# Performance work log

Measured on AMD Instinct MI355X. Metric: run time of the kernel, lower is better.

Reference implementation:

```python
import jax, jax.numpy as jnp
import numpy as np

G = 8           # graphs
NBG = 1024      # blocks per graph
APB = 4         # atoms per block
NC = 1          # coord channels
HID = 512
ES = 64
K = 9
L = 3
NLVL = 50
NB = G * NBG
NU = NB * APB
NUM_BLOCK, NUM_ATOM, NUM_POS = 25, 16, 16
BIG = 1e9


def _cumsum_ids(seg_lengths, n):
    # faithful to torch: zeros, mark segment starts via cumsum(lengths)[:-1], cumsum
    ids = jnp.zeros((n,), jnp.int32).at[jnp.cumsum(seg_lengths)[:-1]].set(1)
    return jnp.cumsum(ids)


def setup_inputs() -> dict:
    key = jax.random.key(0)
    ks = jax.random.split(key, 18)
    s = 0.02
    return {
        'Z': 3.0 * jax.random.normal(ks[0], (NU, NC, 3), jnp.float32),
        'B': jax.random.randint(ks[1], (NB,), 0, NUM_BLOCK),
        'A': jax.random.randint(ks[2], (NU,), 0, NUM_ATOM),
        'atom_positions': jax.random.randint(ks[3], (NU,), 0, NUM_POS),
        'block_lengths': jnp.full((NB,), APB, jnp.int32),
        'lengths': jnp.full((G,), NBG, jnp.int32),
        'segment_ids': jax.random.randint(ks[4], (NB,), 0, 2),
        'noise': jax.random.normal(ks[5], (NU, NC, 3), jnp.float32),
        'noise_level': jax.random.randint(ks[6], (G,), 0, NLVL),
        'sigmas': jnp.asarray(np.exp(np.linspace(np.log(10.0), np.log(0.01), NLVL)), jnp.float32),
        'atom_emb': s * jax.random.normal(ks[7], (NUM_ATOM, HID), jnp.float32),
        'pos_emb': s * jax.random.normal(ks[8], (NUM_POS, HID), jnp.float32),
        'block_emb': s * jax.random.normal(ks[9], (NUM_BLOCK, HID), jnp.float32),
        'edge_emb': s * jax.random.normal(ks[10], (2, ES), jnp.float32),
        'Wm': s * jax.random.normal(ks[11], (L, HID, HID), jnp.float32),
        'We': s * jax.random.normal(ks[12], (L, ES, HID), jnp.float32),
        'Wu': s * jax.random.normal(ks[13], (L, HID, HID), jnp.float32),
        'wz': s * jax.random.normal(ks[14], (L, HID), jnp.float32),
        'W1': s * jax.random.normal(ks[15], (HID, HID), jnp.float32),
        'b1': jnp.zeros((HID,), jnp.float32),
        'W2': s * jax.random.normal(ks[16], (HID, 1), jnp.float32),
    }


def _forward(Z, B, A, atom_positions, block_lengths, lengths, segment_ids,
             noise, noise_level, sigmas, atom_emb, pos_emb, block_emb, edge_emb,
             Wm, We, Wu, wz, W1, b1, W2):
    nb, nu, g = B.shape[0], A.shape[0], lengths.shape[0]
    nbg, apb = nb // g, nu // nb
    batch_id = _cumsum_ids(lengths, nb)        # [Nb]
    block_id = _cumsum_ids(block_lengths, nu)  # [Nu]

    # perturb: Z + noise * sigma[noise_level[graph]]
    used = sigmas[noise_level][batch_id][block_id]          # [Nu]
    Zp = Z + noise * used[:, None, None]                    # [Nu, NC, 3]

    # block embedding: atom + position + block-type
    H0 = atom_emb[A] + pos_emb[atom_positions] + block_emb[B][block_id]  # [Nu, H]

    # edges: fully connect -> split intra/inter by segment -> knn by min atom-pair distance
    xa = Zp.reshape(g, nbg * apb * NC, 3)
    sq = jnp.sum(xa * xa, axis=-1)
    d2 = sq[:, :, None] + sq[:, None, :] - 2.0 * jnp.einsum('gnd,gmd->gnm', xa, xa)
    D = d2.reshape(g, nbg, apb * NC, nbg, apb * NC).min(axis=(2, 4))     # [g, nbg, nbg]
    seg = segment_ids.reshape(g, nbg)
    same = seg[:, :, None] == seg[:, None, :]
    eye = jnp.eye(nbg, dtype=bool)[None]
    _, idx_intra = jax.lax.top_k(-jnp.where(same & ~eye, D, BIG), K)     # [g, nbg, K]
    _, idx_inter = jax.lax.top_k(-jnp.where(~same, D, BIG), K)
    off = (jnp.arange(g, dtype=jnp.int32) * nbg)[:, None, None]
    dst_loc = jnp.broadcast_to(jnp.arange(nbg, dtype=jnp.int32)[None, :, None] + off, (g, nbg, K))
    src = jnp.concatenate([(idx_intra + off).reshape(-1), (idx_inter + off).reshape(-1)])
    dst = jnp.concatenate([dst_loc.reshape(-1), dst_loc.reshape(-1)])
    eattr = edge_emb[jnp.concatenate([jnp.zeros(g * nbg * K, jnp.int32), jnp.ones(g * nbg * K, jnp.int32)])]

    # encoder (GET surrogate): block-level equivariant message passing
    h = jax.ops.segment_sum(H0, block_id, num_segments=nb) / apb                    # [Nb, H]
    Zb0 = jax.ops.segment_sum(Zp.mean(axis=1), block_id, num_segments=nb) / apb    # [Nb, 3]
    Zb = Zb0
    for l in range(Wm.shape[0]):
        m = jax.nn.silu((h[src] + h[dst]) @ Wm[l] + eattr @ We[l])                  # [E, H]
        h = h + jax.nn.silu(jax.ops.segment_sum(m, dst, num_segments=nb) @ Wu[l])
        coef = jnp.tanh(m @ wz[l])                                                  # [E]
        Zb = Zb + jax.ops.segment_sum((Zb[src] - Zb[dst]) * coef[:, None], dst, num_segments=nb) / (2 * K)
    pred_Z = Zp + (Zb - Zb0)[block_id][:, None, :]
    unit_repr = H0 + h[block_id]
    block_repr = h
    graph_repr = jax.ops.segment_sum(h, batch_id, num_segments=g)

    # energy head: SiLU -> Linear -> SiLU -> Linear(no bias), summed per graph
    e = jax.nn.silu(jax.nn.silu(block_repr) @ W1 + b1) @ W2                         # [Nb, 1]
    pred_energy = jax.ops.segment_sum(e[:, 0], batch_id, num_segments=g)            # [g]

    pred_noise = pred_Z - Zp
    per_unit = jnp.sum((pred_noise - noise) ** 2, axis=(-1, -2))                    # [Nu]
    nl = jax.ops.segment_sum(per_unit, batch_id[block_id], num_segments=g)
    loss = 0.5 * nl.mean()
    return pred_energy, pred_noise, unit_repr, block_repr, graph_repr, loss


def reference(Z, B, A, atom_positions, block_lengths, lengths, segment_ids,
              noise, noise_level, sigmas, atom_emb, pos_emb, block_emb, edge_emb,
              Wm, We, Wu, wz, W1, b1, W2):
    return _forward(Z, B, A, atom_positions, block_lengths, lengths, segment_ids,
                    noise, noise_level, sigmas, atom_emb, pos_emb, block_emb, edge_emb,
                    Wm, We, Wu, wz, W1, b1, W2)
```

## Files before the change

kernel.cpp:

```cpp
#include <hip/hip_runtime.h>
#include <hip/hip_bf16.h>

typedef __bf16 bf16;
typedef __bf16 bf16x2 __attribute__((ext_vector_type(2)));
typedef __bf16 bf16x8 __attribute__((ext_vector_type(8)));
typedef float floatx4 __attribute__((ext_vector_type(4)));
typedef float floatx2 __attribute__((ext_vector_type(2)));

__device__ __forceinline__ float silu_f(float x) {
    float e = __expf(-x);
    return x * __builtin_amdgcn_rcpf(1.0f + e);
}

__device__ __forceinline__ float2 unpack_bf2(unsigned v) {
    float2 r;
    r.x = __uint_as_float(v << 16);
    r.y = __uint_as_float(v & 0xFFFF0000u);
    return r;
}

__device__ __forceinline__ void unpack8(const bf16* p, float* o) {
    uint4 u = *(const uint4*)p;
    float2 a = unpack_bf2(u.x); o[0]=a.x; o[1]=a.y;
    float2 b = unpack_bf2(u.y); o[2]=b.x; o[3]=b.y;
    float2 c = unpack_bf2(u.z); o[4]=c.x; o[5]=c.y;
    float2 d = unpack_bf2(u.w); o[6]=d.x; o[7]=d.y;
}

__device__ __forceinline__ void gll16(const bf16* g, bf16* l) {
    __builtin_amdgcn_global_load_lds((const __attribute__((address_space(1))) void*)g,
                                     (__attribute__((address_space(3))) void*)l, 16, 0, 0);
}

__global__ __launch_bounds__(256) void init_kernel(
    const float* __restrict__ Z, const float* __restrict__ noise,
    const int* __restrict__ nl, const float* __restrict__ sig,
    const int* __restrict__ Aarr, const int* __restrict__ posa, const int* __restrict__ Barr,
    const float* __restrict__ atom_emb, const float* __restrict__ pos_emb,
    const float* __restrict__ block_emb,
    const float* __restrict__ Wm,
    float* __restrict__ Zp, float* __restrict__ Zb0, float* __restrict__ Zb,
    float* __restrict__ hf, bf16* __restrict__ hb,
    bf16* __restrict__ WmT)
{
    __shared__ float zsh[12];
    __shared__ float tile[32][33];
    int bid = blockIdx.x, tid = threadIdx.x;
    if (bid < 8192) {
        int b = bid, g = b >> 10;
        if (tid < 12) {
            float sg = sig[nl[g]];
            int idx = b*12 + tid;
            float zp = Z[idx] + noise[idx]*sg;
            Zp[idx] = zp;
            zsh[tid] = zp;
        }
        __syncthreads();
        if (tid < 3) {
            float v = 0.25f*(zsh[tid] + zsh[3+tid] + zsh[6+tid] + zsh[9+tid]);
            Zb0[b*3+tid] = v; Zb[b*3+tid] = v;
        }
        int ai[4], pi[4];
        #pragma unroll
        for (int a = 0; a < 4; a++) { ai[a] = Aarr[b*4+a]*512; pi[a] = posa[b*4+a]*512; }
        int bb = Barr[b]*512;
        #pragma unroll
        for (int cc = 0; cc < 2; cc++) {
            int c = tid + cc*256;
            float s = 0.0f;
            #pragma unroll
            for (int a = 0; a < 4; a++) s += atom_emb[ai[a]+c] + pos_emb[pi[a]+c];
            s = 0.25f*s + block_emb[bb+c];
            hf[(size_t)b*512+c] = s;
            hb[(size_t)b*512+c] = (bf16)s;
        }
        return;
    }
    int rem = bid - 8192;
    int bx = rem & 15, by = rem >> 4;
    int tx = tid & 31, ty = tid >> 5;
    #pragma unroll
    for (int i = 0; i < 32; i += 8)
        tile[ty+i][tx] = Wm[(size_t)(by*32+ty+i)*512 + bx*32+tx];
    __syncthreads();
    #pragma unroll
    for (int i = 0; i < 32; i += 8)
        WmT[(size_t)(bx*32+ty+i)*512 + by*32+tx] = (bf16)tile[tx][ty+i];
}

__device__ void knn_body(int kb, const float* __restrict__ Zp, const int* __restrict__ seg,
                         int* __restrict__ nbr) {
    int wid = threadIdx.x >> 6;
    int lane = threadIdx.x & 63;
    int r = ((kb & 7) << 10) + ((kb >> 3) << 2) + wid;
    int g = r >> 10;
    int il = r & 1023;
    int base = g << 10;
    int segr = seg[r];
    float za[4][3];
    #pragma unroll
    for (int a = 0; a < 4; a++)
        #pragma unroll
        for (int d = 0; d < 3; d++)
            za[a][d] = Zp[r*12 + a*3 + d];
    floatx2 ax[4], ay[4], az[4];
    #pragma unroll
    for (int a = 0; a < 4; a++) {
        ax[a] = (floatx2){za[a][0], za[a][0]};
        ay[a] = (floatx2){za[a][1], za[a][1]};
        az[a] = (floatx2){za[a][2], za[a][2]};
    }
    float dist[16];
    unsigned smask = 0;
    #pragma unroll
    for (int t = 0; t < 16; t++) {
        int jb = base + t*64 + lane;
        const float4* p = (const float4*)(Zp + (size_t)jb*12);
        float4 v0 = p[0], v1 = p[1], v2 = p[2];
        floatx2 bx0 = {v0.x, v0.w}, by0 = {v0.y, v1.x}, bz0 = {v0.z, v1.y};
        floatx2 bx1 = {v1.z, v2.y}, by1 = {v1.w, v2.z}, bz1 = {v2.x, v2.w};
        floatx2 mn = {3.0e38f, 3.0e38f};
        #pragma unroll
        for (int a = 0; a < 4; a++) {
            floatx2 dx = ax[a] - bx0, dy = ay[a] - by0, dz = az[a] - bz0;
            floatx2 dd = dx*dx + dy*dy + dz*dz;
            mn.x = fminf(mn.x, dd.x); mn.y = fminf(mn.y, dd.y);
            dx = ax[a] - bx1; dy = ay[a] - by1; dz = az[a] - bz1;
            dd = dx*dx + dy*dy + dz*dz;
            mn.x = fminf(mn.x, dd.x); mn.y = fminf(mn.y, dd.y);
        }
        dist[t] = fminf(mn.x, mn.y);
        if (seg[jb] == segr) smask |= (1u << t);
    }
    const float INF = 3.0e38f;
    for (int phase = 0; phase < 2; phase++) {
        float wd[16];
        #pragma unroll
        for (int t = 0; t < 16; t++) {
            bool ok = (phase == 0) ? (((smask >> t) & 1u) && (t*64 + lane != il))
                                   : (!((smask >> t) & 1u));
            wd[t] = ok ? dist[t] : INF;
        }
        for (int it = 0; it < 9; it++) {
            float bd = wd[0]; int bt = 0;
            #pragma unroll
            for (int t = 1; t < 16; t++) { if (wd[t] < bd) { bd = wd[t]; bt = t; } }
            float mv = bd;
            #pragma unroll
            for (int off = 32; off >= 1; off >>= 1) mv = fminf(mv, __shfl_xor(mv, off, 64));
            unsigned long long msk = __ballot(bd == mv);
            int wl = __ffsll(msk) - 1;
            int wt = __shfl(bt, wl, 64);
            if (lane == 0) nbr[r*18 + phase*9 + it] = base + wt*64 + wl;
            bool amwin = (lane == wl);
            #pragma unroll
            for (int t = 0; t < 16; t++) if (amwin && t == wt) wd[t] = INF;
        }
    }
}

template<int PIPE>
__device__ void gemm_body(const bf16* __restrict__ A, const bf16* __restrict__ BT,
                          bf16* __restrict__ Pb, float* __restrict__ hf,
                          bf16* __restrict__ hb, bf16* __restrict__ shp,
                          const float* __restrict__ b1, const float* __restrict__ W2,
                          float* __restrict__ out_e,
                          float* __restrict__ Zb, const float* __restrict__ zacc,
                          const float* __restrict__ Zb0, const float* __restrict__ noise,
                          float* __restrict__ out_pn, float* __restrict__ out_loss,
                          float* __restrict__ out_gr,
                          int mode, int bid)
{
    constexpr int NBUF = PIPE ? 3 : 1;
    __shared__ alignas(16) bf16 sA[NBUF*128*32];
    __shared__ alignas(16) bf16 sB[NBUF*64*32];
    __shared__ float grbuf[4][32];
    __shared__ float lsh[4];
    __shared__ float ered[4];
    int mt = bid & 63, nt = bid >> 6;
    int m0 = mt*128, n0 = nt*64;
    int tid = threadIdx.x, lane = tid & 63, w = tid >> 6;
    int wm = w & 1, wn = w >> 1;
    int lm = lane & 15, q = lane >> 4;

    int pA0 = w*128 + lane, pA1 = pA0 + 64, pB = w*64 + lane;
    int rA0 = pA0 >> 2, qA0 = (pA0 & 3) ^ ((rA0 >> 1) & 3);
    int rA1 = pA1 >> 2, qA1 = (pA1 & 3) ^ ((rA1 >> 1) & 3);
    int rB  = pB  >> 2, qB  = (pB  & 3) ^ ((rB  >> 1) & 3);
    const bf16* gA0 = A  + (size_t)(m0 + rA0)*512 + qA0*8;
    const bf16* gA1 = A  + (size_t)(m0 + rA1)*512 + qA1*8;
    const bf16* gB  = BT + (size_t)(n0 + rB )*512 + qB*8;
    int dA0 = (w*128)*8, dA1 = (w*128 + 64)*8, dB = (w*64)*8;

    int swq = (q ^ ((lm >> 1) & 3)) * 8;
    int offA[4], offB[2];
    #pragma unroll
    for (int tm = 0; tm < 4; tm++) offA[tm] = (wm*64 + tm*16 + lm)*32 + swq;
    #pragma unroll
    for (int tn = 0; tn < 2; tn++) offB[tn] = (wn*32 + tn*16 + lm)*32 + swq;

    floatx4 zv = {0.0f, 0.0f, 0.0f, 0.0f};
    floatx4 acc[4][2];
    #pragma unroll
    for (int i = 0; i < 4; i++)
        #pragma unroll
        for (int j = 0; j < 2; j++) acc[i][j] = zv;

    if constexpr (PIPE == 0) {
        for (int k0 = 0; k0 < 512; k0 += 32) {
            gll16(gA0 + k0, sA + dA0);
            gll16(gA1 + k0, sA + dA1);
            gll16(gB  + k0, sB + dB);
            __syncthreads();
            bf16x8 af[4], bfr[2];
            #pragma unroll
            for (int tm = 0; tm < 4; tm++) af[tm] = *(const bf16x8*)(sA + offA[tm]);
            #pragma unroll
            for (int tn = 0; tn < 2; tn++) bfr[tn] = *(const bf16x8*)(sB + offB[tn]);
            #pragma unroll
            for (int tm = 0; tm < 4; tm++)
                #pragma unroll
                for (int tn = 0; tn < 2; tn++)
                    acc[tm][tn] = __builtin_amdgcn_mfma_f32_16x16x32_bf16(af[tm], bfr[tn], acc[tm][tn], 0, 0, 0);
            __syncthreads();
        }
    } else {
        gll16(gA0,      sA + dA0);
        gll16(gA1,      sA + dA1);
        gll16(gB,       sB + dB);
        gll16(gA0 + 32, sA + 4096 + dA0);
        gll16(gA1 + 32, sA + 4096 + dA1);
        gll16(gB  + 32, sB + 2048 + dB);
        #pragma unroll
        for (int t = 0; t < 16; t++) {
            const int cur = t % 3;
            if (t < 14) {
                const int k0 = (t + 2) * 32;
                const int nb = (t + 2) % 3;
                gll16(gA0 + k0, sA + nb*4096 + dA0);
                gll16(gA1 + k0, sA + nb*4096 + dA1);
                gll16(gB  + k0, sB + nb*2048 + dB);
                asm volatile("s_waitcnt vmcnt(6)" ::: "memory");
            } else if (t == 14) {
                asm volatile("s_waitcnt vmcnt(3)" ::: "memory");
            } else {
                asm volatile("s_waitcnt vmcnt(0)" ::: "memory");
            }
            __builtin_amdgcn_s_barrier();
            asm volatile("" ::: "memory");
            const bf16* a_ = sA + cur*4096;
            const bf16* b_ = sB + cur*2048;
            bf16x8 af[4], bfr[2];
            #pragma unroll
            for (int tm = 0; tm < 4; tm++) af[tm] = *(const bf16x8*)(a_ + offA[tm]);
            #pragma unroll
            for (int tn = 0; tn < 2; tn++) bfr[tn] = *(const bf16x8*)(b_ + offB[tn]);
            #pragma unroll
            for (int tm = 0; tm < 4; tm++)
                #pragma unroll
                for (int tn = 0; tn < 2; tn++)
                    acc[tm][tn] = __builtin_amdgcn_mfma_f32_16x16x32_bf16(af[tm], bfr[tn], acc[tm][tn], 0, 0, 0);
            asm volatile("" ::: "memory");
            __builtin_amdgcn_s_barrier();
        }
    }

    if (mode == 1 && nt == 0) {
        int o = m0*3 + tid;
        Zb[o] += zacc[o] * (1.0f/18.0f);
        if (tid < 128) {
            int o2 = m0*3 + 256 + tid;
            Zb[o2] += zacc[o2] * (1.0f/18.0f);
        }
    }

    if (mode == 2) {
        float esum = 0.0f;
        #pragma unroll
        for (int tn = 0; tn < 2; tn++) {
            int col = n0 + wn*32 + tn*16 + lm;
            float bb = b1[col];
            float w2 = W2[col];
            #pragma unroll
            for (int tm = 0; tm < 4; tm++)
                #pragma unroll
                for (int rr = 0; rr < 4; rr++)
                    esum += silu_f(acc[tm][tn][rr] + bb) * w2;
        }
        #pragma unroll
        for (int off = 32; off >= 1; off >>= 1) esum += __shfl_xor(esum, off, 64);
        if (lane == 0) ered[w] = esum;
        __syncthreads();
        if (tid == 0) {
            float tot = ered[0] + ered[1] + ered[2] + ered[3];
            atomicAdd(&out_e[m0 >> 10], tot);
        }
        return;
    }

    float colsum[2] = {0.0f, 0.0f};
    #pragma unroll
    for (int tm = 0; tm < 4; tm++) {
        #pragma unroll
        for (int tn = 0; tn < 2; tn++) {
            #pragma unroll
            for (int rr = 0; rr < 4; rr++) {
                int row = m0 + wm*64 + tm*16 + q*4 + rr;
                int col = n0 + wn*32 + tn*16 + lm;
                size_t o = (size_t)row*512 + col;
                float v = acc[tm][tn][rr];
                if (mode == 0) {
                    Pb[o] = (bf16)v;
                } else {
                    float nh = hf[o] + silu_f(v);
                    hf[o] = nh;
                    colsum[tn] += nh;
                    if (shp) shp[o] = (bf16)silu_f(nh);
                    else     hb[o] = (bf16)nh;
                }
            }
        }
    }

    if (mode == 1 && shp) {
        #pragma unroll
        for (int tn = 0; tn < 2; tn++) {
            float v = colsum[tn];
            v += __shfl_xor(v, 16, 64);
            v += __shfl_xor(v, 32, 64);
            if (q == 0) grbuf[w][tn*16 + lm] = v;
        }
        __syncthreads();
        if (((w & 1) == 0) && lane < 32) {
            float tot = grbuf[w][lane] + grbuf[w + 1][lane];
            int col = n0 + (w >> 1)*32 + lane;
            atomicAdd(&out_gr[(m0 >> 10)*512 + col], tot);
        }
        if (nt == 0) {
            float per2 = 0.0f;
            #pragma unroll
            for (int j = 0; j < 2; j++) {
                int u = m0*4 + tid*2 + j;
                int b = u >> 2;
                #pragma unroll
                for (int d = 0; d < 3; d++) {
                    float dv = Zb[b*3 + d] - Zb0[b*3 + d];
                    out_pn[(size_t)u*3 + d] = dv;
                    float e = dv - noise[(size_t)u*3 + d];
                    per2 += e*e;
                }
            }
            #pragma unroll
            for (int off = 32; off >= 1; off >>= 1) per2 += __shfl_xor(per2, off, 64);
            if (lane == 0) lsh[w] = per2;
            __syncthreads();
            if (tid == 0)
                atomicAdd(out_loss, (lsh[0]+lsh[1]+lsh[2]+lsh[3]) * (1.0f/16.0f));
        }
    }
}

template<int MODE>
__global__ __launch_bounds__(256) void gemm_mode_kernel(const bf16* __restrict__ A, const bf16* __restrict__ BT,
                                                        bf16* __restrict__ Pb, float* __restrict__ hf,
                                                        bf16* __restrict__ hb, bf16* __restrict__ shp,
                                                        const float* __restrict__ b1, const float* __restrict__ W2,
                                                        float* __restrict__ out_e,
                                                        float* __restrict__ Zb, const float* __restrict__ zacc,
                                                        const float* __restrict__ Zb0, const float* __restrict__ noise,
                                                        float* __restrict__ out_pn, float* __restrict__ out_loss,
                                                        float* __restrict__ out_gr) {
    gemm_body<1>(A, BT, Pb, hf, hb, shp, b1, W2, out_e, Zb, zacc,
                 Zb0, noise, out_pn, out_loss, out_gr, MODE, blockIdx.x);
}

__global__ __launch_bounds__(256) void knn_pgemm0_kernel(const bf16* __restrict__ hb,
                                                         const bf16* __restrict__ WmT,
                                                         bf16* __restrict__ Pb,
                                                         const float* __restrict__ Zp,
                                                         const int* __restrict__ seg,
                                                         int* __restrict__ nbr,
                                                         const float* __restrict__ Wm,
                                                         const float* __restrict__ Wu,
                                                         const float* __restrict__ W1,
                                                         bf16* __restrict__ WmTw,
                                                         bf16* __restrict__ WuT,
                                                         bf16* __restrict__ W1T,
                                                         const float* __restrict__ edge_emb,
                                                         const float* __restrict__ We,
                                                         float* __restrict__ ebias,
                                                         float* __restrict__ out_gr,
                                                         float* __restrict__ out_e,
                                                         float* __restrict__ out_loss) {
    __shared__ float ttile[32][33];
    int bid = blockIdx.x, tid = threadIdx.x;
    if (bid < 512) {
        gemm_body<0>(hb, WmT, Pb, nullptr, nullptr, nullptr, nullptr, nullptr, nullptr,
                     nullptr, nullptr, nullptr, nullptr, nullptr, nullptr, nullptr, 0, bid);
        return;
    }
    if (bid < 2560) {
        knn_body(bid - 512, Zp, seg, nbr);
        return;
    }
    int tb = bid - 2560;
    if (tb < 1536) {
        int z = 1 + (tb >> 8), rem = tb & 255;
        int bx = rem & 15, by = rem >> 4;
        int tx = tid & 31, ty = tid >> 5;
        const float* src; bf16* dst;
        if (z < 3)      { src = Wm + (size_t)z*262144;     dst = WmTw + (size_t)z*262144; }
        else if (z < 6) { src = Wu + (size_t)(z-3)*262144; dst = WuT + (size_t)(z-3)*262144; }
        else            { src = W1;                        dst = W1T; }
        #pragma unroll
        for (int i = 0; i < 32; i += 8)
            ttile[ty+i][tx] = src[(size_t)(by*32+ty+i)*512 + bx*32+tx];
        __syncthreads();
        #pragma unroll
        for (int i = 0; i < 32; i += 8)
            dst[(size_t)(bx*32+ty+i)*512 + by*32+tx] = (bf16)ttile[tx][ty+i];
        return;
    }
    tb -= 1536;
    if (tb < 12) {
        int gid = tb*256 + tid;
        int l = gid >> 10, t = (gid >> 9) & 1, c = gid & 511;
        float s = 0.0f;
        #pragma unroll 8
        for (int e = 0; e < 64; e++)
            s += edge_emb[t*64 + e] * We[(size_t)(l*64 + e)*512 + c];
        ebias[gid] = s;
        return;
    }
    tb -= 12;
    int k = tb*256 + tid;
    if (k < 4096) out_gr[k] = 0.0f;
    else if (k < 4104) out_e[k-4096] = 0.0f;
    else if (k == 4104) out_loss[0] = 0.0f;
}

__global__ __launch_bounds__(256) void edge_kernel(const bf16* __restrict__ Pb, const float* __restrict__ ebias,
                                                   const float* __restrict__ wz, const float* __restrict__ Zb,
                                                   const int* __restrict__ nbr, bf16* __restrict__ msum,
                                                   float* __restrict__ zacc) {
    int bid = blockIdx.x, tid = threadIdx.x;
    int lane = tid & 63, wid = tid >> 6;
    int b = ((bid & 7) << 10) | ((bid >> 3) << 2) | wid;
    __shared__ int srcs[4][18];
    if (tid < 72) {
        int w2 = tid / 18, e2 = tid - w2*18;
        int bb = ((bid & 7) << 10) | ((bid >> 3) << 2) | w2;
        srcs[w2][e2] = nbr[bb*18 + e2];
    }
    __syncthreads();
    int c0 = lane << 3;
    float pd[8], eb0[8], eb1[8], wv[8];
    unpack8(Pb + (size_t)b*512 + c0, pd);
    *(float4*)(eb0)   = *(const float4*)(ebias + c0);
    *(float4*)(eb0+4) = *(const float4*)(ebias + c0 + 4);
    *(float4*)(eb1)   = *(const float4*)(ebias + 512 + c0);
    *(float4*)(eb1+4) = *(const float4*)(ebias + 512 + c0 + 4);
    *(float4*)(wv)    = *(const float4*)(wz + c0);
    *(float4*)(wv+4)  = *(const float4*)(wz + c0 + 4);
    float ms[8];
    #pragma unroll
    for (int j = 0; j < 8; j++) ms[j] = 0.0f;
    float pdot[18];
    #pragma unroll
    for (int e = 0; e < 18; e++) {
        int s = srcs[wid][e];
        float pv[8];
        unpack8(Pb + (size_t)s*512 + c0, pv);
        float dot = 0.0f;
        #pragma unroll
        for (int j = 0; j < 8; j++) {
            float base = (e < 9) ? eb0[j] : eb1[j];
            float m = silu_f(pv[j] + pd[j] + base);
            ms[j] += m;
            dot += m * wv[j];
        }
        pdot[e] = dot;
    }
    bf16x8 mp;
    #pragma unroll
    for (int j = 0; j < 8; j++) mp[j] = (bf16)ms[j];
    *(bf16x8*)(msum + (size_t)b*512 + c0) = mp;
    #pragma unroll
    for (int e = 0; e < 18; e++) {
        float v = pdot[e];
        #pragma unroll
        for (int off = 32; off >= 1; off >>= 1) v += __shfl_xor(v, off, 64);
        pdot[e] = v;
    }
    float dotv = 0.0f;
    #pragma unroll
    for (int e = 0; e < 18; e++) dotv = (lane == e) ? pdot[e] : dotv;
    float coef = tanhf(dotv);
    float t3[3] = {0.0f, 0.0f, 0.0f};
    if (lane < 18) {
        int se = srcs[wid][lane];
        #pragma unroll
        for (int d = 0; d < 3; d++)
            t3[d] = (Zb[se*3 + d] - Zb[b*3 + d]) * coef;
    }
    #pragma unroll
    for (int off = 16; off >= 1; off >>= 1) {
        t3[0] += __shfl_xor(t3[0], off, 64);
        t3[1] += __shfl_xor(t3[1], off, 64);
        t3[2] += __shfl_xor(t3[2], off, 64);
    }
    if (lane == 0) {
        zacc[b*3 + 0] = t3[0];
        zacc[b*3 + 1] = t3[1];
        zacc[b*3 + 2] = t3[2];
    }
}

__global__ __launch_bounds__(256) void unitrepr_kernel(const int* __restrict__ Aarr, const int* __restrict__ posa,
                                                       const int* __restrict__ Barr,
                                                       const float* __restrict__ atom_emb, const float* __restrict__ pos_emb,
                                                       const float* __restrict__ block_emb,
                                                       const float* __restrict__ hf, float* __restrict__ out_ur) {
    int gid = blockIdx.x*256 + threadIdx.x;
    int u = gid >> 7, c = (gid & 127) << 2, b = u >> 2;
    float4 va = *(const float4*)(atom_emb + (size_t)Aarr[u]*512 + c);
    float4 vp = *(const float4*)(pos_emb + (size_t)posa[u]*512 + c);
    float4 vb = *(const float4*)(block_emb + (size_t)Barr[b]*512 + c);
    float4 vh = *(const float4*)(hf + (size_t)b*512 + c);
    float4 o;
    o.x = va.x + vp.x + vb.x + vh.x;
    o.y = va.y + vp.y + vb.y + vh.y;
    o.z = va.z + vp.z + vb.z + vh.z;
    o.w = va.w + vp.w + vb.w + vh.w;
    *(float4*)(out_ur + (size_t)u*512 + c) = o;
}

extern "C" void kernel_launch(void* const* d_in, const int* in_sizes, int n_in,
                              void* d_out, int out_size, void* d_ws, size_t ws_size,
                              hipStream_t stream) {
    const float* Z         = (const float*)d_in[0];
    const int*   B         = (const int*)d_in[1];
    const int*   A         = (const int*)d_in[2];
    const int*   ap        = (const int*)d_in[3];
    const int*   seg       = (const int*)d_in[6];
    const float* noise     = (const float*)d_in[7];
    const int*   nl        = (const int*)d_in[8];
    const float* sig       = (const float*)d_in[9];
    const float* atom_emb  = (const float*)d_in[10];
    const float* pos_emb   = (const float*)d_in[11];
    const float* block_emb = (const float*)d_in[12];
    const float* edge_emb  = (const float*)d_in[13];
    const float* Wm        = (const float*)d_in[14];
    const float* We        = (const float*)d_in[15];
    const float* Wu        = (const float*)d_in[16];
    const float* wz        = (const float*)d_in[17];
    const float* W1        = (const float*)d_in[18];
    const float* b1        = (const float*)d_in[19];
    const float* W2        = (const float*)d_in[20];
    (void)in_sizes; (void)n_in; (void)d_ws; (void)ws_size; (void)out_size;

    float* out = (float*)d_out;
    const size_t o1 = 8, o2 = 98312, o3 = 16875528, o4 = 21069832, o5 = 21073928;
    float* out_e    = out;
    float* out_pn   = out + o1;
    float* out_ur   = out + o2;
    float* hf       = out + o3;
    float* out_gr   = out + o4;
    float* out_loss = out + o5;

    char* arena = (char*)(out + o2);
    bf16*  Pb   = (bf16*)(arena);
    bf16*  msum = (bf16*)(arena + 16777216);
    bf16*  sh   = (bf16*)(arena + 25165824);
    bf16*  hb   = (bf16*)(arena + 33554432);
    float* Zp   = (float*)(arena + 41943040);
    float* Zb0  = (float*)(arena + 42336256);
    float* Zb   = (float*)(arena + 42434560);
    float* zacc = (float*)(arena + 42532864);
    int*   nbr  = (int*)  (arena + 42631168);
    bf16*  WmT  = (bf16*) (arena + 43220992);
    bf16*  WuT  = (bf16*) (arena + 44793856);
    bf16*  W1T  = (bf16*) (arena + 46366720);
    float* ebias= (float*)(arena + 46891008);

    init_kernel<<<8192 + 256, 256, 0, stream>>>(
        Z, noise, nl, sig, A, ap, B, atom_emb, pos_emb, block_emb,
        Wm, Zp, Zb0, Zb, hf, hb, WmT);

    knn_pgemm0_kernel<<<512 + 2048 + 1536 + 12 + 17, 256, 0, stream>>>(
        hb, WmT, Pb, Zp, seg, nbr,
        Wm, Wu, W1, WmT, WuT, W1T,
        edge_emb, We, ebias, out_gr, out_e, out_loss);

    for (int l = 0; l < 3; l++) {
        if (l > 0)
            gemm_mode_kernel<0><<<512, 256, 0, stream>>>(hb, WmT + (size_t)l*262144, Pb,
                                                 nullptr, nullptr, nullptr, nullptr, nullptr, nullptr,
                                                 nullptr, nullptr, nullptr, nullptr, nullptr, nullptr, nullptr);
        edge_kernel<<<2048, 256, 0, stream>>>(Pb, ebias + l*1024, wz + l*512, Zb, nbr, msum, zacc);
        gemm_mode_kernel<1><<<512, 256, 0, stream>>>(msum, WuT + (size_t)l*262144, nullptr,
                                             hf, hb, (l == 2) ? sh : nullptr, nullptr, nullptr, nullptr,
                                             Zb, zacc, Zb0, noise, out_pn, out_loss, out_gr);
    }
    gemm_mode_kernel<2><<<512, 256, 0, stream>>>(sh, W1T, nullptr, nullptr, nullptr, nullptr,
                                         b1, W2, out_e, nullptr, nullptr,
                                         nullptr, nullptr, nullptr, nullptr, nullptr);
    unitrepr_kernel<<<16384, 256, 0, stream>>>(A, ap, B, atom_emb, pos_emb, block_emb, hf, out_ur);
}
```

Measured before the change: 428.2 us.

## Use 64-row GEMM tiles with doubled grid and drop triple-buffered pipeline

The standalone GEMM kernels now use a 64-row M tile instead of 128 and launch 1024 blocks instead of 512, giving the 256 CUs more blocks to spread across. The triple-buffered async-load pipeline is replaced by the simple single-buffer load/sync/MFMA loop, which also cuts LDS use and may raise occupancy. Loses latency hiding from prefetching and reloads each B tile twice as often in exchange for better CU fill. Epilogue loops are generalized to the tile size.

```diff
diff --git a/kernel.cpp b/kernel.cpp
--- a/kernel.cpp
+++ b/kernel.cpp
@@ -159,7 +159,7 @@
     }
 }
 
-template<int PIPE>
+template<int BM>
 __device__ void gemm_body(const bf16* __restrict__ A, const bf16* __restrict__ BT,
                           bf16* __restrict__ Pb, float* __restrict__ hf,
                           bf16* __restrict__ hb, bf16* __restrict__ shp,
@@ -171,107 +171,69 @@
                           float* __restrict__ out_gr,
                           int mode, int bid)
 {
-    constexpr int NBUF = PIPE ? 3 : 1;
-    __shared__ alignas(16) bf16 sA[NBUF*128*32];
-    __shared__ alignas(16) bf16 sB[NBUF*64*32];
+    constexpr int TM = BM / 32;
+    constexpr int AL = BM / 64;
+    constexpr int MT_MASK = (8192 / BM) - 1;
+    constexpr int NT_SHIFT = (BM == 128) ? 6 : 7;
+    __shared__ alignas(16) bf16 sA[BM*32];
+    __shared__ alignas(16) bf16 sB[64*32];
     __shared__ float grbuf[4][32];
     __shared__ float lsh[4];
     __shared__ float ered[4];
-    int mt = bid & 63, nt = bid >> 6;
-    int m0 = mt*128, n0 = nt*64;
+    int mt = bid & MT_MASK, nt = bid >> NT_SHIFT;
+    int m0 = mt*BM, n0 = nt*64;
     int tid = threadIdx.x, lane = tid & 63, w = tid >> 6;
     int wm = w & 1, wn = w >> 1;
     int lm = lane & 15, q = lane >> 4;
 
-    int pA0 = w*128 + lane, pA1 = pA0 + 64, pB = w*64 + lane;
-    int rA0 = pA0 >> 2, qA0 = (pA0 & 3) ^ ((rA0 >> 1) & 3);
-    int rA1 = pA1 >> 2, qA1 = (pA1 & 3) ^ ((rA1 >> 1) & 3);
-    int rB  = pB  >> 2, qB  = (pB  & 3) ^ ((rB  >> 1) & 3);
-    const bf16* gA0 = A  + (size_t)(m0 + rA0)*512 + qA0*8;
-    const bf16* gA1 = A  + (size_t)(m0 + rA1)*512 + qA1*8;
-    const bf16* gB  = BT + (size_t)(n0 + rB )*512 + qB*8;
-    int dA0 = (w*128)*8, dA1 = (w*128 + 64)*8, dB = (w*64)*8;
+    const bf16* gA[AL]; int dA[AL];
+    #pragma unroll
+    for (int j = 0; j < AL; j++) {
+        int pA = w*BM + j*64 + lane;
+        int rA = pA >> 2, qA = (pA & 3) ^ ((rA >> 1) & 3);
+        gA[j] = A + (size_t)(m0 + rA)*512 + qA*8;
+        dA[j] = (w*BM + j*64)*8;
+    }
+    int pB = w*64 + lane;
+    int rB = pB >> 2, qB = (pB & 3) ^ ((rB >> 1) & 3);
+    const bf16* gB = BT + (size_t)(n0 + rB)*512 + qB*8;
+    int dB = (w*64)*8;
 
     int swq = (q ^ ((lm >> 1) & 3)) * 8;
-    int offA[4], offB[2];
-    #pragma unroll
-    for (int tm = 0; tm < 4; tm++) offA[tm] = (wm*64 + tm*16 + lm)*32 + swq;
+    int offA[TM], offB[2];
+    #pragma unroll
+    for (int tm = 0; tm < TM; tm++) offA[tm] = (wm*(BM/2) + tm*16 + lm)*32 + swq;
     #pragma unroll
     for (int tn = 0; tn < 2; tn++) offB[tn] = (wn*32 + tn*16 + lm)*32 + swq;
 
     floatx4 zv = {0.0f, 0.0f, 0.0f, 0.0f};
-    floatx4 acc[4][2];
-    #pragma unroll
-    for (int i = 0; i < 4; i++)
+    floatx4 acc[TM][2];
+    #pragma unroll
+    for (int i = 0; i < TM; i++)
         #pragma unroll
         for (int j = 0; j < 2; j++) acc[i][j] = zv;
 
-    if constexpr (PIPE == 0) {
-        for (int k0 = 0; k0 < 512; k0 += 32) {
-            gll16(gA0 + k0, sA + dA0);
-            gll16(gA1 + k0, sA + dA1);
-            gll16(gB  + k0, sB + dB);
-            __syncthreads();
-            bf16x8 af[4], bfr[2];
-            #pragma unroll
-            for (int tm = 0; tm < 4; tm++) af[tm] = *(const bf16x8*)(sA + offA[tm]);
-            #pragma unroll
-            for (int tn = 0; tn < 2; tn++) bfr[tn] = *(const bf16x8*)(sB + offB[tn]);
-            #pragma unroll
-            for (int tm = 0; tm < 4; tm++)
-                #pragma unroll
-                for (int tn = 0; tn < 2; tn++)
-                    acc[tm][tn] = __builtin_amdgcn_mfma_f32_16x16x32_bf16(af[tm], bfr[tn], acc[tm][tn], 0, 0, 0);
-            __syncthreads();
-        }
-    } else {
-        gll16(gA0,      sA + dA0);
-        gll16(gA1,      sA + dA1);
-        gll16(gB,       sB + dB);
-        gll16(gA0 + 32, sA + 4096 + dA0);
-        gll16(gA1 + 32, sA + 4096 + dA1);
-        gll16(gB  + 32, sB + 2048 + dB);
-        #pragma unroll
-        for (int t = 0; t < 16; t++) {
-            const int cur = t % 3;
-            if (t < 14) {
-                const int k0 = (t + 2) * 32;
-                const int nb = (t + 2) % 3;
-                gll16(gA0 + k0, sA + nb*4096 + dA0);
-                gll16(gA1 + k0, sA + nb*4096 + dA1);
-                gll16(gB  + k0, sB + nb*2048 + dB);
-                asm volatile("s_waitcnt vmcnt(6)" ::: "memory");
-            } else if (t == 14) {
-                asm volatile("s_waitcnt vmcnt(3)" ::: "memory");
-            } else {
-                asm volatile("s_waitcnt vmcnt(0)" ::: "memory");
-            }
-            __builtin_amdgcn_s_barrier();
-            asm volatile("" ::: "memory");
-            const bf16* a_ = sA + cur*4096;
-            const bf16* b_ = sB + cur*2048;
-            bf16x8 af[4], bfr[2];
-            #pragma unroll
-            for (int tm = 0; tm < 4; tm++) af[tm] = *(const bf16x8*)(a_ + offA[tm]);
-            #pragma unroll
-            for (int tn = 0; tn < 2; tn++) bfr[tn] = *(const bf16x8*)(b_ + offB[tn]);
-            #pragma unroll
-            for (int tm = 0; tm < 4; tm++)
-                #pragma unroll
-                for (int tn = 0; tn < 2; tn++)
-                    acc[tm][tn] = __builtin_amdgcn_mfma_f32_16x16x32_bf16(af[tm], bfr[tn], acc[tm][tn], 0, 0, 0);
-            asm volatile("" ::: "memory");
-            __builtin_amdgcn_s_barrier();
-        }
+    for (int k0 = 0; k0 < 512; k0 += 32) {
+        #pragma unroll
+        for (int j = 0; j < AL; j++) gll16(gA[j] + k0, sA + dA[j]);
+        gll16(gB + k0, sB + dB);
+        __syncthreads();
+        bf16x8 af[TM], bfr[2];
+        #pragma unroll
+        for (int tm = 0; tm < TM; tm++) af[tm] = *(const bf16x8*)(sA + offA[tm]);
+        #pragma unroll
+        for (int tn = 0; tn < 2; tn++) bfr[tn] = *(const bf16x8*)(sB + offB[tn]);
+        #pragma unroll
+        for (int tm = 0; tm < TM; tm++)
+            #pragma unroll
+            for (int tn = 0; tn < 2; tn++)
+                acc[tm][tn] = __builtin_amdgcn_mfma_f32_16x16x32_bf16(af[tm], bfr[tn], acc[tm][tn], 0, 0, 0);
+        __syncthreads();
     }
 
     if (mode == 1 && nt == 0) {
-        int o = m0*3 + tid;
-        Zb[o] += zacc[o] * (1.0f/18.0f);
-        if (tid < 128) {
-            int o2 = m0*3 + 256 + tid;
-            Zb[o2] += zacc[o2] * (1.0f/18.0f);
-        }
+        for (int o = tid; o < BM*3; o += 256)
+            Zb[m0*3 + o] += zacc[m0*3 + o] * (1.0f/18.0f);
     }
 
     if (mode == 2) {
@@ -282,7 +244,7 @@
             float bb = b1[col];
             float w2 = W2[col];
             #pragma unroll
-            for (int tm = 0; tm < 4; tm++)
+            for (int tm = 0; tm < TM; tm++)
                 #pragma unroll
                 for (int rr = 0; rr < 4; rr++)
                     esum += silu_f(acc[tm][tn][rr] + bb) * w2;
@@ -300,12 +262,12 @@
 
     float colsum[2] = {0.0f, 0.0f};
     #pragma unroll
-    for (int tm = 0; tm < 4; tm++) {
+    for (int tm = 0; tm < TM; tm++) {
         #pragma unroll
         for (int tn = 0; tn < 2; tn++) {
             #pragma unroll
             for (int rr = 0; rr < 4; rr++) {
-                int row = m0 + wm*64 + tm*16 + q*4 + rr;
+                int row = m0 + wm*(BM/2) + tm*16 + q*4 + rr;
                 int col = n0 + wn*32 + tn*16 + lm;
                 size_t o = (size_t)row*512 + col;
                 float v = acc[tm][tn][rr];
@@ -338,9 +300,8 @@
         }
         if (nt == 0) {
             float per2 = 0.0f;
-            #pragma unroll
-            for (int j = 0; j < 2; j++) {
-                int u = m0*4 + tid*2 + j;
+            for (int uu = tid; uu < BM*4; uu += 256) {
+                int u = m0*4 + uu;
                 int b = u >> 2;
                 #pragma unroll
                 for (int d = 0; d < 3; d++) {
@@ -370,8 +331,8 @@
                                                         const float* __restrict__ Zb0, const float* __restrict__ noise,
                                                         float* __restrict__ out_pn, float* __restrict__ out_loss,
                                                         float* __restrict__ out_gr) {
-    gemm_body<1>(A, BT, Pb, hf, hb, shp, b1, W2, out_e, Zb, zacc,
-                 Zb0, noise, out_pn, out_loss, out_gr, MODE, blockIdx.x);
+    gemm_body<64>(A, BT, Pb, hf, hb, shp, b1, W2, out_e, Zb, zacc,
+                  Zb0, noise, out_pn, out_loss, out_gr, MODE, blockIdx.x);
 }
 
 __global__ __launch_bounds__(256) void knn_pgemm0_kernel(const bf16* __restrict__ hb,
@@ -395,8 +356,8 @@
     __shared__ float ttile[32][33];
     int bid = blockIdx.x, tid = threadIdx.x;
     if (bid < 512) {
-        gemm_body<0>(hb, WmT, Pb, nullptr, nullptr, nullptr, nullptr, nullptr, nullptr,
-                     nullptr, nullptr, nullptr, nullptr, nullptr, nullptr, nullptr, 0, bid);
+        gemm_body<128>(hb, WmT, Pb, nullptr, nullptr, nullptr, nullptr, nullptr, nullptr,
+                       nullptr, nullptr, nullptr, nullptr, nullptr, nullptr, nullptr, 0, bid);
         return;
     }
     if (bid < 2560) {
@@ -594,15 +555,15 @@
 
     for (int l = 0; l < 3; l++) {
         if (l > 0)
-            gemm_mode_kernel<0><<<512, 256, 0, stream>>>(hb, WmT + (size_t)l*262144, Pb,
+            gemm_mode_kernel<0><<<1024, 256, 0, stream>>>(hb, WmT + (size_t)l*262144, Pb,
                                                  nullptr, nullptr, nullptr, nullptr, nullptr, nullptr,
                                                  nullptr, nullptr, nullptr, nullptr, nullptr, nullptr, nullptr);
         edge_kernel<<<2048, 256, 0, stream>>>(Pb, ebias + l*1024, wz + l*512, Zb, nbr, msum, zacc);
-        gemm_mode_kernel<1><<<512, 256, 0, stream>>>(msum, WuT + (size_t)l*262144, nullptr,
+        gemm_mode_kernel<1><<<1024, 256, 0, stream>>>(msum, WuT + (size_t)l*262144, nullptr,
                                              hf, hb, (l == 2) ? sh : nullptr, nullptr, nullptr, nullptr,
                                              Zb, zacc, Zb0, noise, out_pn, out_loss, out_gr);
     }
-    gemm_mode_kernel<2><<<512, 256, 0, stream>>>(sh, W1T, nullptr, nullptr, nullptr, nullptr,
+    gemm_mode_kernel<2><<<1024, 256, 0, stream>>>(sh, W1T, nullptr, nullptr, nullptr, nullptr,
                                          b1, W2, out_e, nullptr, nullptr,
                                          nullptr, nullptr, nullptr, nullptr, nullptr);
     unitrepr_kernel<<<16384, 256, 0, stream>>>(A, ap, B, atom_emb, pos_emb, block_emb, hf, out_ur);
```

Result: slower. 437.3 us (+2.1%).

## Replace LDS-staged GEMM with per-wave register-direct 32x32 tile GEMM

Applied to the files above, without the earlier changes.

The per-layer GEMMs drop the shared-memory triple-buffered 128x64 block tile. Each wave now computes a 32x32 output tile, loading MFMA fragments straight from global memory into registers with a two-stage software prefetch, and the grid doubles to 1024 blocks. Epilogue reductions (graph sums, loss, energy) switch from LDS plus block barriers to per-wave atomics. This removes LDS traffic and barriers and raises parallelism, but loses operand reuse across waves, so global/L2 load traffic grows and the number of atomics rises.

```diff
diff --git a/kernel.cpp b/kernel.cpp
--- a/kernel.cpp
+++ b/kernel.cpp
@@ -159,24 +159,11 @@
     }
 }
 
-template<int PIPE>
-__device__ void gemm_body(const bf16* __restrict__ A, const bf16* __restrict__ BT,
-                          bf16* __restrict__ Pb, float* __restrict__ hf,
-                          bf16* __restrict__ hb, bf16* __restrict__ shp,
-                          const float* __restrict__ b1, const float* __restrict__ W2,
-                          float* __restrict__ out_e,
-                          float* __restrict__ Zb, const float* __restrict__ zacc,
-                          const float* __restrict__ Zb0, const float* __restrict__ noise,
-                          float* __restrict__ out_pn, float* __restrict__ out_loss,
-                          float* __restrict__ out_gr,
-                          int mode, int bid)
+__device__ void gemm0_body(const bf16* __restrict__ A, const bf16* __restrict__ BT,
+                           bf16* __restrict__ Pb, int bid)
 {
-    constexpr int NBUF = PIPE ? 3 : 1;
-    __shared__ alignas(16) bf16 sA[NBUF*128*32];
-    __shared__ alignas(16) bf16 sB[NBUF*64*32];
-    __shared__ float grbuf[4][32];
-    __shared__ float lsh[4];
-    __shared__ float ered[4];
+    __shared__ alignas(16) bf16 sA[128*32];
+    __shared__ alignas(16) bf16 sB[64*32];
     int mt = bid & 63, nt = bid >> 6;
     int m0 = mt*128, n0 = nt*64;
     int tid = threadIdx.x, lane = tid & 63, w = tid >> 6;
@@ -206,110 +193,129 @@
         #pragma unroll
         for (int j = 0; j < 2; j++) acc[i][j] = zv;
 
-    if constexpr (PIPE == 0) {
-        for (int k0 = 0; k0 < 512; k0 += 32) {
-            gll16(gA0 + k0, sA + dA0);
-            gll16(gA1 + k0, sA + dA1);
-            gll16(gB  + k0, sB + dB);
-            __syncthreads();
-            bf16x8 af[4], bfr[2];
-            #pragma unroll
-            for (int tm = 0; tm < 4; tm++) af[tm] = *(const bf16x8*)(sA + offA[tm]);
-            #pragma unroll
-            for (int tn = 0; tn < 2; tn++) bfr[tn] = *(const bf16x8*)(sB + offB[tn]);
-            #pragma unroll
-            for (int tm = 0; tm < 4; tm++)
-                #pragma unroll
-                for (int tn = 0; tn < 2; tn++)
-                    acc[tm][tn] = __builtin_amdgcn_mfma_f32_16x16x32_bf16(af[tm], bfr[tn], acc[tm][tn], 0, 0, 0);
-            __syncthreads();
-        }
-    } else {
-        gll16(gA0,      sA + dA0);
-        gll16(gA1,      sA + dA1);
-        gll16(gB,       sB + dB);
-        gll16(gA0 + 32, sA + 4096 + dA0);
-        gll16(gA1 + 32, sA + 4096 + dA1);
-        gll16(gB  + 32, sB + 2048 + dB);
-        #pragma unroll
-        for (int t = 0; t < 16; t++) {
-            const int cur = t % 3;
-            if (t < 14) {
-                const int k0 = (t + 2) * 32;
-                const int nb = (t + 2) % 3;
-                gll16(gA0 + k0, sA + nb*4096 + dA0);
-                gll16(gA1 + k0, sA + nb*4096 + dA1);
-                gll16(gB  + k0, sB + nb*2048 + dB);
-                asm volatile("s_waitcnt vmcnt(6)" ::: "memory");
-            } else if (t == 14) {
-                asm volatile("s_waitcnt vmcnt(3)" ::: "memory");
-            } else {
-                asm volatile("s_waitcnt vmcnt(0)" ::: "memory");
+    for (int k0 = 0; k0 < 512; k0 += 32) {
+        gll16(gA0 + k0, sA + dA0);
+        gll16(gA1 + k0, sA + dA1);
+        gll16(gB  + k0, sB + dB);
+        __syncthreads();
+        bf16x8 af[4], bfr[2];
+        #pragma unroll
+        for (int tm = 0; tm < 4; tm++) af[tm] = *(const bf16x8*)(sA + offA[tm]);
+        #pragma unroll
+        for (int tn = 0; tn < 2; tn++) bfr[tn] = *(const bf16x8*)(sB + offB[tn]);
+        #pragma unroll
+        for (int tm = 0; tm < 4; tm++)
+            #pragma unroll
+            for (int tn = 0; tn < 2; tn++)
+                acc[tm][tn] = __builtin_amdgcn_mfma_f32_16x16x32_bf16(af[tm], bfr[tn], acc[tm][tn], 0, 0, 0);
+        __syncthreads();
+    }
+
+    #pragma unroll
+    for (int tm = 0; tm < 4; tm++)
+        #pragma unroll
+        for (int tn = 0; tn < 2; tn++)
+            #pragma unroll
+            for (int rr = 0; rr < 4; rr++) {
+                int row = m0 + wm*64 + tm*16 + q*4 + rr;
+                int col = n0 + wn*32 + tn*16 + lm;
+                Pb[(size_t)row*512 + col] = (bf16)acc[tm][tn][rr];
             }
-            __builtin_amdgcn_s_barrier();
-            asm volatile("" ::: "memory");
-            const bf16* a_ = sA + cur*4096;
-            const bf16* b_ = sB + cur*2048;
-            bf16x8 af[4], bfr[2];
-            #pragma unroll
-            for (int tm = 0; tm < 4; tm++) af[tm] = *(const bf16x8*)(a_ + offA[tm]);
-            #pragma unroll
-            for (int tn = 0; tn < 2; tn++) bfr[tn] = *(const bf16x8*)(b_ + offB[tn]);
-            #pragma unroll
-            for (int tm = 0; tm < 4; tm++)
-                #pragma unroll
-                for (int tn = 0; tn < 2; tn++)
-                    acc[tm][tn] = __builtin_amdgcn_mfma_f32_16x16x32_bf16(af[tm], bfr[tn], acc[tm][tn], 0, 0, 0);
-            asm volatile("" ::: "memory");
-            __builtin_amdgcn_s_barrier();
-        }
-    }
-
-    if (mode == 1 && nt == 0) {
-        int o = m0*3 + tid;
-        Zb[o] += zacc[o] * (1.0f/18.0f);
-        if (tid < 128) {
-            int o2 = m0*3 + 256 + tid;
-            Zb[o2] += zacc[o2] * (1.0f/18.0f);
-        }
-    }
-
-    if (mode == 2) {
+}
+
+template<int MODE>
+__global__ __launch_bounds__(256) void wgemm_kernel(
+    const bf16* __restrict__ A, const bf16* __restrict__ BT,
+    bf16* __restrict__ Pb, float* __restrict__ hf,
+    bf16* __restrict__ hb, bf16* __restrict__ shp,
+    const float* __restrict__ b1, const float* __restrict__ W2,
+    float* __restrict__ out_e,
+    float* __restrict__ Zb, const float* __restrict__ zacc,
+    const float* __restrict__ Zb0, const float* __restrict__ noise,
+    float* __restrict__ out_pn, float* __restrict__ out_loss,
+    float* __restrict__ out_gr)
+{
+    int tid = threadIdx.x, lane = tid & 63, w = tid >> 6;
+    int wid = blockIdx.x*4 + w;
+    int wm = wid >> 4, wn = wid & 15;
+    int r0 = wm*32, c0 = wn*32;
+    int lm = lane & 15, q = lane >> 4;
+
+    const bf16* pa0 = A  + (size_t)(r0 + lm)*512      + q*8;
+    const bf16* pa1 = A  + (size_t)(r0 + 16 + lm)*512 + q*8;
+    const bf16* pb0 = BT + (size_t)(c0 + lm)*512      + q*8;
+    const bf16* pb1 = BT + (size_t)(c0 + 16 + lm)*512 + q*8;
+
+    floatx4 zv = {0.0f, 0.0f, 0.0f, 0.0f};
+    floatx4 acc[2][2] = {{zv, zv}, {zv, zv}};
+
+    bf16x8 aE0 = *(const bf16x8*)(pa0);
+    bf16x8 aE1 = *(const bf16x8*)(pa1);
+    bf16x8 bE0 = *(const bf16x8*)(pb0);
+    bf16x8 bE1 = *(const bf16x8*)(pb1);
+    #pragma unroll
+    for (int t = 0; t < 8; t++) {
+        const int kO = t*64 + 32;
+        bf16x8 aO0 = *(const bf16x8*)(pa0 + kO);
+        bf16x8 aO1 = *(const bf16x8*)(pa1 + kO);
+        bf16x8 bO0 = *(const bf16x8*)(pb0 + kO);
+        bf16x8 bO1 = *(const bf16x8*)(pb1 + kO);
+        acc[0][0] = __builtin_amdgcn_mfma_f32_16x16x32_bf16(aE0, bE0, acc[0][0], 0, 0, 0);
+        acc[0][1] = __builtin_amdgcn_mfma_f32_16x16x32_bf16(aE0, bE1, acc[0][1], 0, 0, 0);
+        acc[1][0] = __builtin_amdgcn_mfma_f32_16x16x32_bf16(aE1, bE0, acc[1][0], 0, 0, 0);
+        acc[1][1] = __builtin_amdgcn_mfma_f32_16x16x32_bf16(aE1, bE1, acc[1][1], 0, 0, 0);
+        if (t < 7) {
+            const int kE = t*64 + 64;
+            aE0 = *(const bf16x8*)(pa0 + kE);
+            aE1 = *(const bf16x8*)(pa1 + kE);
+            bE0 = *(const bf16x8*)(pb0 + kE);
+            bE1 = *(const bf16x8*)(pb1 + kE);
+        }
+        acc[0][0] = __builtin_amdgcn_mfma_f32_16x16x32_bf16(aO0, bO0, acc[0][0], 0, 0, 0);
+        acc[0][1] = __builtin_amdgcn_mfma_f32_16x16x32_bf16(aO0, bO1, acc[0][1], 0, 0, 0);
+        acc[1][0] = __builtin_amdgcn_mfma_f32_16x16x32_bf16(aO1, bO0, acc[1][0], 0, 0, 0);
+        acc[1][1] = __builtin_amdgcn_mfma_f32_16x16x32_bf16(aO1, bO1, acc[1][1], 0, 0, 0);
+    }
+
+    if (MODE == 2) {
         float esum = 0.0f;
         #pragma unroll
         for (int tn = 0; tn < 2; tn++) {
-            int col = n0 + wn*32 + tn*16 + lm;
+            int col = c0 + tn*16 + lm;
             float bb = b1[col];
             float w2 = W2[col];
             #pragma unroll
-            for (int tm = 0; tm < 4; tm++)
+            for (int tm = 0; tm < 2; tm++)
                 #pragma unroll
                 for (int rr = 0; rr < 4; rr++)
                     esum += silu_f(acc[tm][tn][rr] + bb) * w2;
         }
         #pragma unroll
         for (int off = 32; off >= 1; off >>= 1) esum += __shfl_xor(esum, off, 64);
-        if (lane == 0) ered[w] = esum;
-        __syncthreads();
-        if (tid == 0) {
-            float tot = ered[0] + ered[1] + ered[2] + ered[3];
-            atomicAdd(&out_e[m0 >> 10], tot);
-        }
+        if (lane == 0) atomicAdd(&out_e[wm >> 5], esum);
         return;
     }
 
+    if (MODE == 1 && wn == 0) {
+        #pragma unroll
+        for (int o = 0; o < 2; o++) {
+            int i = o*64 + lane;
+            if (i < 96) Zb[r0*3 + i] += zacc[r0*3 + i] * (1.0f/18.0f);
+        }
+    }
+
     float colsum[2] = {0.0f, 0.0f};
     #pragma unroll
-    for (int tm = 0; tm < 4; tm++) {
+    for (int tm = 0; tm < 2; tm++) {
         #pragma unroll
         for (int tn = 0; tn < 2; tn++) {
             #pragma unroll
             for (int rr = 0; rr < 4; rr++) {
-                int row = m0 + wm*64 + tm*16 + q*4 + rr;
-                int col = n0 + wn*32 + tn*16 + lm;
+                int row = r0 + tm*16 + q*4 + rr;
+                int col = c0 + tn*16 + lm;
                 size_t o = (size_t)row*512 + col;
                 float v = acc[tm][tn][rr];
-                if (mode == 0) {
+                if (MODE == 0) {
                     Pb[o] = (bf16)v;
                 } else {
                     float nh = hf[o] + silu_f(v);
@@ -322,25 +328,20 @@
         }
     }
 
-    if (mode == 1 && shp) {
+    if (MODE == 1 && shp) {
+        int g = wm >> 5;
         #pragma unroll
         for (int tn = 0; tn < 2; tn++) {
             float v = colsum[tn];
             v += __shfl_xor(v, 16, 64);
             v += __shfl_xor(v, 32, 64);
-            if (q == 0) grbuf[w][tn*16 + lm] = v;
-        }
-        __syncthreads();
-        if (((w & 1) == 0) && lane < 32) {
-            float tot = grbuf[w][lane] + grbuf[w + 1][lane];
-            int col = n0 + (w >> 1)*32 + lane;
-            atomicAdd(&out_gr[(m0 >> 10)*512 + col], tot);
-        }
-        if (nt == 0) {
+            if (q == 0) atomicAdd(&out_gr[g*512 + c0 + tn*16 + lm], v);
+        }
+        if (wn == 0) {
             float per2 = 0.0f;
             #pragma unroll
             for (int j = 0; j < 2; j++) {
-                int u = m0*4 + tid*2 + j;
+                int u = r0*4 + lane*2 + j;
                 int b = u >> 2;
                 #pragma unroll
                 for (int d = 0; d < 3; d++) {
@@ -352,26 +353,9 @@
             }
             #pragma unroll
             for (int off = 32; off >= 1; off >>= 1) per2 += __shfl_xor(per2, off, 64);
-            if (lane == 0) lsh[w] = per2;
-            __syncthreads();
-            if (tid == 0)
-                atomicAdd(out_loss, (lsh[0]+lsh[1]+lsh[2]+lsh[3]) * (1.0f/16.0f));
-        }
-    }
-}
-
-template<int MODE>
-__global__ __launch_bounds__(256) void gemm_mode_kernel(const bf16* __restrict__ A, const bf16* __restrict__ BT,
-                                                        bf16* __restrict__ Pb, float* __restrict__ hf,
-                                                        bf16* __restrict__ hb, bf16* __restrict__ shp,
-                                                        const float* __restrict__ b1, const float* __restrict__ W2,
-                                                        float* __restrict__ out_e,
-                                                        float* __restrict__ Zb, const float* __restrict__ zacc,
-                                                        const float* __restrict__ Zb0, const float* __restrict__ noise,
-                                                        float* __restrict__ out_pn, float* __restrict__ out_loss,
-                                                        float* __restrict__ out_gr) {
-    gemm_body<1>(A, BT, Pb, hf, hb, shp, b1, W2, out_e, Zb, zacc,
-                 Zb0, noise, out_pn, out_loss, out_gr, MODE, blockIdx.x);
+            if (lane == 0) atomicAdd(out_loss, per2 * (1.0f/16.0f));
+        }
+    }
 }
 
 __global__ __launch_bounds__(256) void knn_pgemm0_kernel(const bf16* __restrict__ hb,
@@ -395,8 +379,7 @@
     __shared__ float ttile[32][33];
     int bid = blockIdx.x, tid = threadIdx.x;
     if (bid < 512) {
-        gemm_body<0>(hb, WmT, Pb, nullptr, nullptr, nullptr, nullptr, nullptr, nullptr,
-                     nullptr, nullptr, nullptr, nullptr, nullptr, nullptr, nullptr, 0, bid);
+        gemm0_body(hb, WmT, Pb, bid);
         return;
     }
     if (bid < 2560) {
@@ -594,15 +577,15 @@
 
     for (int l = 0; l < 3; l++) {
         if (l > 0)
-            gemm_mode_kernel<0><<<512, 256, 0, stream>>>(hb, WmT + (size_t)l*262144, Pb,
+            wgemm_kernel<0><<<1024, 256, 0, stream>>>(hb, WmT + (size_t)l*262144, Pb,
                                                  nullptr, nullptr, nullptr, nullptr, nullptr, nullptr,
                                                  nullptr, nullptr, nullptr, nullptr, nullptr, nullptr, nullptr);
         edge_kernel<<<2048, 256, 0, stream>>>(Pb, ebias + l*1024, wz + l*512, Zb, nbr, msum, zacc);
-        gemm_mode_kernel<1><<<512, 256, 0, stream>>>(msum, WuT + (size_t)l*262144, nullptr,
+        wgemm_kernel<1><<<1024, 256, 0, stream>>>(msum, WuT + (size_t)l*262144, nullptr,
                                              hf, hb, (l == 2) ? sh : nullptr, nullptr, nullptr, nullptr,
                                              Zb, zacc, Zb0, noise, out_pn, out_loss, out_gr);
     }
-    gemm_mode_kernel<2><<<512, 256, 0, stream>>>(sh, W1T, nullptr, nullptr, nullptr, nullptr,
+    wgemm_kernel<2><<<1024, 256, 0, stream>>>(sh, W1T, nullptr, nullptr, nullptr, nullptr,
                                          b1, W2, out_e, nullptr, nullptr,
                                          nullptr, nullptr, nullptr, nullptr, nullptr);
     unitrepr_kernel<<<16384, 256, 0, stream>>>(A, ap, B, atom_emb, pos_emb, block_emb, hf, out_ur);
```

Measured after the change: 572.0 us. 1.34x slower.
